# Optimization experiments

Measured on AMD Instinct MI355X. Metric: run time of the kernel, lower is better.

Reference implementation:

```python
import jax, jax.numpy as jnp
import numpy as np

B, DIN, H = 16384, 512, 512
K = 7  # LC_i1, LC_i2, LC_f1, LC_f2, LC_o, LC_z (gate nets, idx 0..5), LC_d (decay net, idx 6)


def setup_inputs() -> dict:
    key = jax.random.key(0)
    ks = jax.random.split(key, 8)
    s1 = 1.0 / np.sqrt(DIN)
    s2 = 1.0 / np.sqrt(H)
    return {
        "hx": jax.random.normal(ks[0], (B, DIN), jnp.float32),
        "cx1": jax.random.normal(ks[1], (B, H), jnp.float32),
        "cx2": jax.random.normal(ks[2], (B, H), jnp.float32),
        # stacked params for the 7 sub-networks (same structure: Linear(DIN,H) -> Linear(H,H))
        "W1": jax.random.uniform(ks[3], (K, H, DIN), jnp.float32, -s1, s1),
        "b1": jax.random.uniform(ks[4], (K, H), jnp.float32, -s1, s1),
        "W2": jax.random.uniform(ks[5], (K, H, H), jnp.float32, -s2, s2),
        "b2": jax.random.uniform(ks[6], (K, H), jnp.float32, -s2, s2),
    }


def reference(hx, cx1, cx2, W1, b1, W2, b2):
    # layer 1 for all 7 nets at once: [K, B, H]
    h1 = jnp.einsum('bd,khd->kbh', hx, W1) + b1[:, None, :]
    # gate nets use tanh, decay net uses softplus
    a1 = jnp.concatenate([jnp.tanh(h1[:6]), jax.nn.softplus(h1[6:])], axis=0)
    # layer 2: [K, B, H]
    h2 = jnp.einsum('kbh,kgh->kbg', a1, W2) + b2[:, None, :]
    gates = jax.nn.sigmoid(jnp.tanh(h2[:6]))  # Gate_network: sigmoid(tanh(.))
    d = jax.nn.softplus(h2[6])                # Decay_network output (decay_coef, side state)
    i1, i2, f1, f2, o, zg = gates
    z = jnp.tanh(zg)                          # z = Tanh(LC_z(hx))
    cy1 = f1 * cx1 + i1 * z                   # side state self.cy1
    cy2 = f2 * cx2 + i2 * z
    return cy2
```

## Files before the change

### kernel.cpp

```cpp
#include <hip/hip_runtime.h>
#include <hip/hip_bf16.h>

typedef __attribute__((ext_vector_type(8))) __bf16 bf16x8;
typedef __attribute__((ext_vector_type(4))) __bf16 bf16x4;
typedef __attribute__((ext_vector_type(4))) float f32x4;

constexpr int M = 16384;
constexpr int K = 512;
constexpr int BK = 32;

__device__ __forceinline__ void async_copy16(const void* gsrc, void* ldst) {
  __builtin_amdgcn_global_load_lds(
      (const __attribute__((address_space(1))) unsigned int*)(gsrc),
      (__attribute__((address_space(3))) unsigned int*)(ldst),
      16, 0, 0);
}

__device__ __forceinline__ float frcp(float x) { return __builtin_amdgcn_rcpf(x); }
__device__ __forceinline__ float ftanh(float x) {
  return 1.0f - 2.0f * frcp(1.0f + __expf(2.0f * x));
}
__device__ __forceinline__ float fsigm(float x) {
  return frcp(1.0f + __expf(-x));
}

template <int LAYER>
__global__ __launch_bounds__(256) void gemm_kernel(
    const __bf16* __restrict__ A,
    const __bf16* __restrict__ W,
    const float* __restrict__ bias,
    __bf16* __restrict__ out)
{
  const int j = blockIdx.z;
  const int mbase = blockIdx.x * 128;
  const int nbase = blockIdx.y * 128;
  const __bf16* Aj = (LAYER == 2) ? (A + (size_t)j * M * K) : A;
  const __bf16* Wj = W + (size_t)j * K * K;

  __shared__ __align__(16) __bf16 smem[17408];

  const int tid  = threadIdx.x;
  const int wid  = tid >> 6;
  const int lane = tid & 63;
  const int wm   = (wid >> 1) * 64;
  const int wn   = (wid & 1) * 64;
  const int srow = wid * 16 + (lane >> 2);
  const int scol = ((lane & 3) ^ ((lane >> 3) & 3)) * 8;
  const int fr   = lane & 15;
  const int kc   = lane >> 4;
  const int sw   = (fr >> 1) & 3;
  const int rowq = kc * 4;

  auto stage = [&](int p, int k0) {
    __bf16* As = smem + p * 8192;
    __bf16* Bs = As + 4096;
#pragma unroll
    for (int r = 0; r < 2; ++r) {
      async_copy16(Aj + (size_t)(mbase + r * 64 + srow) * K + (k0 + scol),
                   (void*)&As[(r * 64 + wid * 16) * BK]);
      async_copy16(Wj + (size_t)(nbase + r * 64 + srow) * K + (k0 + scol),
                   (void*)&Bs[(r * 64 + wid * 16) * BK]);
    }
  };

  f32x4 acc[4][4] = {};

  stage(0, 0);
  int p = 0;
  for (int k0 = 0; k0 < K; k0 += BK) {
    __syncthreads();
    if (k0 + BK < K) stage(p ^ 1, k0 + BK);

    const __bf16* As = smem + p * 8192;
    const __bf16* Bs = As + 4096;
    bf16x8 af[4], bfr[4];
#pragma unroll
    for (int i = 0; i < 4; ++i) {
      af[i]  = *(const bf16x8*)&As[(wm + i * 16 + fr) * BK + ((kc ^ sw) * 8)];
      bfr[i] = *(const bf16x8*)&Bs[(wn + i * 16 + fr) * BK + ((kc ^ sw) * 8)];
    }
#pragma unroll
    for (int mi = 0; mi < 4; ++mi)
#pragma unroll
      for (int ni = 0; ni < 4; ++ni)
        acc[mi][ni] = __builtin_amdgcn_mfma_f32_16x16x32_bf16(
            af[mi], bfr[ni], acc[mi][ni], 0, 0, 0);
    p ^= 1;
  }

  float bv[4];
  const float* bj = bias + (2 * j + 1) * 512 + nbase + wn;
#pragma unroll
  for (int ni = 0; ni < 4; ++ni) bv[ni] = bj[ni * 16 + fr];

  __syncthreads();
#pragma unroll
  for (int mi = 0; mi < 4; ++mi)
#pragma unroll
    for (int ni = 0; ni < 4; ++ni)
#pragma unroll
      for (int r = 0; r < 4; ++r) {
        float v = acc[mi][ni][r] + bv[ni];
        float res;
        if constexpr (LAYER == 1) {
          res = ftanh(v);
        } else {
          res = (j == 2) ? ftanh(fsigm(ftanh(v))) : fsigm(ftanh(v));
        }
        smem[(wm + mi * 16 + rowq + r) * 136 + (wn + ni * 16 + fr)] =
            (__bf16)res;
      }
  __syncthreads();
#pragma unroll
  for (int it = 0; it < 8; ++it) {
    const int s = it * 256 + tid;
    const int row = s >> 4, ch = s & 15;
    bf16x8 v = *(const bf16x8*)&smem[row * 136 + ch * 8];
    *(bf16x8*)&out[(size_t)j * M * 512 + (size_t)(mbase + row) * 512 +
                   (nbase + ch * 8)] = v;
  }
}

__global__ __launch_bounds__(256) void final_kernel(
    const __bf16* __restrict__ gates, const float* __restrict__ cx2,
    float* __restrict__ out)
{
  constexpr size_t NH = (size_t)M * 512;
  const size_t i = ((size_t)blockIdx.x * 256 + threadIdx.x) * 8;
  bf16x8 i2 = *(const bf16x8*)&gates[i];
  bf16x8 f2 = *(const bf16x8*)&gates[NH + i];
  bf16x8 zz = *(const bf16x8*)&gates[2 * NH + i];
  f32x4 c0 = *(const f32x4*)&cx2[i];
  f32x4 c1 = *(const f32x4*)&cx2[i + 4];
#pragma unroll
  for (int h = 0; h < 2; ++h) {
    f32x4 r;
#pragma unroll
    for (int q = 0; q < 4; ++q) {
      const int e = h * 4 + q;
      r[q] = (float)f2[e] * (h ? c1[q] : c0[q]) + (float)i2[e] * (float)zz[e];
    }
    *(f32x4*)&out[i + h * 4] = r;
  }
}

__global__ __launch_bounds__(256) void cvt_hx(const float* __restrict__ src,
                                              __bf16* __restrict__ dst) {
  const size_t i = ((size_t)blockIdx.x * 256 + threadIdx.x) * 4;
  f32x4 v = *(const f32x4*)&src[i];
  *(bf16x4*)&dst[i] = __builtin_convertvector(v, bf16x4);
}

__global__ __launch_bounds__(256) void cvt_w(const float* __restrict__ src,
                                             __bf16* __restrict__ dst) {
  const int j = blockIdx.y;
  const size_t i = ((size_t)blockIdx.x * 256 + threadIdx.x) * 4;
  f32x4 v = *(const f32x4*)&src[(size_t)(2 * j + 1) * 262144 + i];
  *(bf16x4*)&dst[(size_t)j * 262144 + i] = __builtin_convertvector(v, bf16x4);
}

extern "C" void kernel_launch(void* const* d_in, const int* in_sizes, int n_in,
                              void* d_out, int out_size, void* d_ws, size_t ws_size,
                              hipStream_t stream) {
  const float* hx  = (const float*)d_in[0];
  const float* cx2 = (const float*)d_in[2];
  const float* W1  = (const float*)d_in[3];
  const float* b1  = (const float*)d_in[4];
  const float* W2  = (const float*)d_in[5];
  const float* b2  = (const float*)d_in[6];
  float* out = (float*)d_out;

  char* ws = (char*)d_ws;
  __bf16* hxb   = (__bf16*)(ws);
  __bf16* W1b   = (__bf16*)(ws + 16777216);
  __bf16* W2b   = (__bf16*)(ws + 18350080);
  __bf16* a1    = (__bf16*)(ws + 19922944);
  __bf16* gates = (__bf16*)(ws + 70254592);

  cvt_hx<<<8192, 256, 0, stream>>>(hx, hxb);
  cvt_w<<<dim3(256, 3), 256, 0, stream>>>(W1, W1b);
  cvt_w<<<dim3(256, 3), 256, 0, stream>>>(W2, W2b);

  gemm_kernel<1><<<dim3(128, 4, 3), 256, 0, stream>>>(hxb, W1b, b1, a1);
  gemm_kernel<2><<<dim3(128, 4, 3), 256, 0, stream>>>(a1, W2b, b2, gates);

  final_kernel<<<4096, 256, 0, stream>>>(gates, cx2, out);
}
```

Before: 234.0 us.

## Load GEMM weight fragments directly from global into registers and merge conversion kernels

The GEMM kernel stops staging the weight tile through LDS. Each lane now reads its B fragments straight from global memory into registers, prefetching one K-step ahead, while only the activation tile keeps the async global-to-LDS double buffer. This halves LDS traffic and footprint per block, but adds uncoalesced per-lane global loads and extra registers. The three fp32-to-bf16 conversion launches are also combined into a single kernel to save launch overhead.

```diff
diff --git a/kernel.cpp b/kernel.cpp
--- a/kernel.cpp
+++ b/kernel.cpp
@@ -52,39 +52,49 @@
   const int rowq = kc * 4;
 
   auto stage = [&](int p, int k0) {
-    __bf16* As = smem + p * 8192;
-    __bf16* Bs = As + 4096;
-#pragma unroll
-    for (int r = 0; r < 2; ++r) {
+    __bf16* As = smem + p * 4096;
+#pragma unroll
+    for (int r = 0; r < 2; ++r)
       async_copy16(Aj + (size_t)(mbase + r * 64 + srow) * K + (k0 + scol),
                    (void*)&As[(r * 64 + wid * 16) * BK]);
-      async_copy16(Wj + (size_t)(nbase + r * 64 + srow) * K + (k0 + scol),
-                   (void*)&Bs[(r * 64 + wid * 16) * BK]);
-    }
   };
 
+  const __bf16* Wbase = Wj + (size_t)(nbase + wn + fr) * K + kc * 8;
+  auto loadB = [&](int k0, bf16x8* b) {
+#pragma unroll
+    for (int i = 0; i < 4; ++i)
+      b[i] = *(const bf16x8*)&Wbase[(size_t)i * 16 * K + k0];
+  };
+
   f32x4 acc[4][4] = {};
 
   stage(0, 0);
+  bf16x8 bfr[4];
+  loadB(0, bfr);
+
   int p = 0;
   for (int k0 = 0; k0 < K; k0 += BK) {
     __syncthreads();
     if (k0 + BK < K) stage(p ^ 1, k0 + BK);
 
-    const __bf16* As = smem + p * 8192;
-    const __bf16* Bs = As + 4096;
-    bf16x8 af[4], bfr[4];
-#pragma unroll
-    for (int i = 0; i < 4; ++i) {
-      af[i]  = *(const bf16x8*)&As[(wm + i * 16 + fr) * BK + ((kc ^ sw) * 8)];
-      bfr[i] = *(const bf16x8*)&Bs[(wn + i * 16 + fr) * BK + ((kc ^ sw) * 8)];
-    }
+    bf16x8 bnext[4];
+    if (k0 + BK < K) loadB(k0 + BK, bnext);
+
+    const __bf16* As = smem + p * 4096;
+    bf16x8 af[4];
+#pragma unroll
+    for (int i = 0; i < 4; ++i)
+      af[i] = *(const bf16x8*)&As[(wm + i * 16 + fr) * BK + ((kc ^ sw) * 8)];
+
 #pragma unroll
     for (int mi = 0; mi < 4; ++mi)
 #pragma unroll
       for (int ni = 0; ni < 4; ++ni)
         acc[mi][ni] = __builtin_amdgcn_mfma_f32_16x16x32_bf16(
             af[mi], bfr[ni], acc[mi][ni], 0, 0, 0);
+
+#pragma unroll
+    for (int i = 0; i < 4; ++i) bfr[i] = bnext[i];
     p ^= 1;
   }
 
@@ -144,19 +154,30 @@
   }
 }
 
-__global__ __launch_bounds__(256) void cvt_hx(const float* __restrict__ src,
-                                              __bf16* __restrict__ dst) {
-  const size_t i = ((size_t)blockIdx.x * 256 + threadIdx.x) * 4;
+__global__ __launch_bounds__(256) void cvt_all(
+    const float* __restrict__ hx, const float* __restrict__ W1,
+    const float* __restrict__ W2, __bf16* __restrict__ hxb,
+    __bf16* __restrict__ W1b, __bf16* __restrict__ W2b)
+{
+  const int b = blockIdx.x;
+  const float* src;
+  __bf16* dst;
+  size_t i;
+  if (b < 8192) {
+    src = hx; dst = hxb;
+    i = ((size_t)b * 256 + threadIdx.x) * 4;
+  } else {
+    const int bb = (b < 8960) ? (b - 8192) : (b - 8960);
+    const int jj = bb >> 8;
+    const int blk = bb & 255;
+    const size_t off = (size_t)(2 * jj + 1) * 262144;
+    const size_t doff = (size_t)jj * 262144;
+    i = ((size_t)blk * 256 + threadIdx.x) * 4;
+    if (b < 8960) { src = W1 + off; dst = W1b + doff; }
+    else          { src = W2 + off; dst = W2b + doff; }
+  }
   f32x4 v = *(const f32x4*)&src[i];
   *(bf16x4*)&dst[i] = __builtin_convertvector(v, bf16x4);
-}
-
-__global__ __launch_bounds__(256) void cvt_w(const float* __restrict__ src,
-                                             __bf16* __restrict__ dst) {
-  const int j = blockIdx.y;
-  const size_t i = ((size_t)blockIdx.x * 256 + threadIdx.x) * 4;
-  f32x4 v = *(const f32x4*)&src[(size_t)(2 * j + 1) * 262144 + i];
-  *(bf16x4*)&dst[(size_t)j * 262144 + i] = __builtin_convertvector(v, bf16x4);
 }
 
 extern "C" void kernel_launch(void* const* d_in, const int* in_sizes, int n_in,
@@ -177,9 +198,7 @@
   __bf16* a1    = (__bf16*)(ws + 19922944);
   __bf16* gates = (__bf16*)(ws + 70254592);
 
-  cvt_hx<<<8192, 256, 0, stream>>>(hx, hxb);
-  cvt_w<<<dim3(256, 3), 256, 0, stream>>>(W1, W1b);
-  cvt_w<<<dim3(256, 3), 256, 0, stream>>>(W2, W2b);
+  cvt_all<<<9728, 256, 0, stream>>>(hx, W1, W2, hxb, W1b, W2b);
 
   gemm_kernel<1><<<dim3(128, 4, 3), 256, 0, stream>>>(hxb, W1b, b1, a1);
   gemm_kernel<2><<<dim3(128, 4, 3), 256, 0, stream>>>(a1, W2b, b2, gates);
```

Result: slower. 269.5 us (+15.2%).
